# Kernel tuning notes

Measured on AMD Instinct MI355X. Metric: run time of the kernel, lower is better.

## Reference

```python
import jax, jax.numpy as jnp
import numpy as np
import math

DX = DZ = DATTN = DOUT = 1024
LX = LZ = 4096

def setup_inputs() -> dict:
    key = jax.random.key(0)
    ks = jax.random.split(key, 6)
    X = jax.random.normal(ks[0], (DX, LX), dtype=jnp.float32)
    Z = jax.random.normal(ks[1], (DZ, LZ), dtype=jnp.float32)
    mask = jax.random.randint(ks[2], (LZ, LX), 0, 2) > 0  # bool (lz, lx)
    Wq = jax.random.normal(ks[3], (DATTN, DX), dtype=jnp.float32) / math.sqrt(DATTN)
    bq = jnp.zeros((DATTN, 1), dtype=jnp.float32)
    Wk = jax.random.normal(ks[4], (DATTN, DZ), dtype=jnp.float32) / math.sqrt(DATTN)
    bk = jnp.zeros((DATTN, 1), dtype=jnp.float32)
    Wv = jax.random.normal(ks[5], (DOUT, DZ), dtype=jnp.float32) / math.sqrt(DOUT)
    bv = jnp.zeros((DOUT, 1), dtype=jnp.float32)
    return {"X": X, "Z": Z, "mask": mask, "Wq": Wq, "bq": bq,
            "Wk": Wk, "bk": bk, "Wv": Wv, "bv": bv}

def reference(X, Z, mask, Wq, bq, Wk, bk, Wv, bv):
    dattn_sqrt = math.sqrt(Wq.shape[0])
    q = Wq @ X + bq                      # (dattn, lx)
    k = Wk @ Z + bk                      # (dattn, lz)
    v = Wv @ Z + bv                      # (dout, lz)
    score = k.T @ q                      # (lz, lx)
    # masked_fill with -1000 happens BEFORE scaling, matching the original
    score = jnp.where(mask, score, jnp.float32(-1000.0))
    attn = jax.nn.softmax(score / dattn_sqrt, axis=0)  # softmax over lz (dim 0)
    return v @ attn                      # (dout, lx)
```

## Files before the change

### kernel.cpp

```cpp
#include <hip/hip_runtime.h>
#include <hip/hip_bf16.h>
#include <math.h>

constexpr int DXc = 1024;
constexpr int DZc = 1024;
constexpr int LXc = 4096;
constexpr int LZc = 4096;
constexpr int DAc = 1024;
constexpr int DOc = 1024;

typedef __attribute__((ext_vector_type(8))) short bf16x8;
typedef __attribute__((ext_vector_type(4))) float f32x4;

__device__ __forceinline__ ushort f2bf(float f) {
    __hip_bfloat16 h = __float2bfloat16(f);
    return *reinterpret_cast<ushort*>(&h);
}
__device__ __forceinline__ float bflo(unsigned u) {
    return __builtin_bit_cast(float, u << 16);
}
__device__ __forceinline__ float bfhi(unsigned u) {
    return __builtin_bit_cast(float, u & 0xffff0000u);
}

enum BiasMode { BIAS_NONE, BIAS_M, BIAS_N };

template<BiasMode BMODE, bool OUT_BF16, bool SPLIT>
__device__ __forceinline__ void gemm_tile(
    const ushort* __restrict__ A, const ushort* __restrict__ B,
    const float* __restrict__ bias, void* __restrict__ Cv,
    int M, int N, int K, int lda, int ldb, int ldc,
    int m0, int n0, int kbase, int zsplit,
    ushort* As, ushort* Bs)
{
    constexpr int BK = 32;
    const int tid = threadIdx.x;
    const int wv  = tid >> 6;
    const int wm  = (wv >> 1) * 64;
    const int wn  = (wv & 1) * 64;
    const int ln  = tid & 63;
    const int lrow = ln & 15;
    const int quad = ln >> 4;

    const int srow = tid >> 2;
    const int sseg = (tid & 3) * 8;
    const ushort* Ag = A + (size_t)(m0 + srow) * lda + sseg + kbase;
    const ushort* Bg = B + (size_t)(n0 + srow) * ldb + sseg + kbase;
    ushort* AsW = As + wv * 512;
    ushort* BsW = Bs + wv * 512;

    f32x4 acc[4][4] = {};

    for (int k0 = 0; k0 < K; k0 += BK) {
        __syncthreads();
        __builtin_amdgcn_global_load_lds(
            (const __attribute__((address_space(1))) void*)(Ag + k0),
            (__attribute__((address_space(3))) void*)(AsW), 16, 0, 0);
        __builtin_amdgcn_global_load_lds(
            (const __attribute__((address_space(1))) void*)(Ag + (size_t)64 * lda + k0),
            (__attribute__((address_space(3))) void*)(AsW + 2048), 16, 0, 0);
        __builtin_amdgcn_global_load_lds(
            (const __attribute__((address_space(1))) void*)(Bg + k0),
            (__attribute__((address_space(3))) void*)(BsW), 16, 0, 0);
        __builtin_amdgcn_global_load_lds(
            (const __attribute__((address_space(1))) void*)(Bg + (size_t)64 * ldb + k0),
            (__attribute__((address_space(3))) void*)(BsW + 2048), 16, 0, 0);
        __syncthreads();

        bf16x8 af[4], bfr[4];
        #pragma unroll
        for (int t = 0; t < 4; ++t) {
            af[t]  = *reinterpret_cast<const bf16x8*>(&As[(wm + t * 16 + lrow) * BK + quad * 8]);
            bfr[t] = *reinterpret_cast<const bf16x8*>(&Bs[(wn + t * 16 + lrow) * BK + quad * 8]);
        }
        #pragma unroll
        for (int mi = 0; mi < 4; ++mi)
            #pragma unroll
            for (int nj = 0; nj < 4; ++nj)
                acc[mi][nj] = __builtin_amdgcn_mfma_f32_16x16x32_bf16(
                    af[mi], bfr[nj], acc[mi][nj], 0, 0, 0);
    }

    float*  Cf = (float*)Cv + (SPLIT ? (size_t)zsplit * M * ldc : 0);
    ushort* Cb = (ushort*)Cv;
    #pragma unroll
    for (int mi = 0; mi < 4; ++mi) {
        #pragma unroll
        for (int r = 0; r < 4; ++r) {
            const int m = m0 + wm + mi * 16 + quad * 4 + r;
            const float bm = (BMODE == BIAS_M) ? bias[m] : 0.0f;
            #pragma unroll
            for (int nj = 0; nj < 4; ++nj) {
                const int n = n0 + wn + nj * 16 + lrow;
                float v = acc[mi][nj][r] + ((BMODE == BIAS_N) ? bias[n] : bm);
                if (OUT_BF16) Cb[(size_t)m * ldc + n] = f2bf(v);
                else          Cf[(size_t)m * ldc + n] = v;
            }
        }
    }
}

__global__ __launch_bounds__(256)
void proj_kernel(const ushort* __restrict__ XT, const ushort* __restrict__ ZT,
                 const ushort* __restrict__ Wqb, const ushort* __restrict__ Wkb,
                 const ushort* __restrict__ Wvb,
                 const float* __restrict__ bq, const float* __restrict__ bk,
                 const float* __restrict__ bv,
                 ushort* __restrict__ qT, ushort* __restrict__ kT,
                 ushort* __restrict__ vB)
{
    __shared__ __align__(16) ushort As[128 * 32];
    __shared__ __align__(16) ushort Bs[128 * 32];
    int b = blockIdx.x;
    if (b < 256) {
        const int x = b & 7, y = b >> 3;
        gemm_tile<BIAS_N, true, false>(XT, Wqb, bq, qT, LXc, DAc, DXc,
                                       DXc, DXc, DAc, y * 128, x * 128, 0, 0, As, Bs);
    } else if (b < 512) {
        b -= 256;
        const int x = b & 7, y = b >> 3;
        gemm_tile<BIAS_N, true, false>(ZT, Wkb, bk, kT, LZc, DAc, DZc,
                                       DZc, DZc, DAc, y * 128, x * 128, 0, 0, As, Bs);
    } else {
        b -= 512;
        const int x = b & 31, y = b >> 5;
        gemm_tile<BIAS_M, true, false>(Wvb, ZT, bv, vB, DOc, LZc, DZc,
                                       DZc, DZc, LZc, y * 128, x * 128, 0, 0, As, Bs);
    }
}

__global__ __launch_bounds__(256)
void score_kernel(const ushort* __restrict__ qT, const ushort* __restrict__ kT,
                  ushort* __restrict__ sTb)
{
    __shared__ __align__(16) ushort As[128 * 32];
    __shared__ __align__(16) ushort Bs[128 * 32];
    const int b = blockIdx.x;
    const int x = b & 31, y = b >> 5;
    gemm_tile<BIAS_NONE, true, false>(qT, kT, nullptr, sTb, LXc, LZc, DAc,
                                      DAc, DAc, LZc, y * 128, x * 128, 0, 0, As, Bs);
}

__global__ __launch_bounds__(256)
void out_kernel(const ushort* __restrict__ vB, const ushort* __restrict__ sTb,
                float* __restrict__ P)
{
    __shared__ __align__(16) ushort As[128 * 32];
    __shared__ __align__(16) ushort Bs[128 * 32];
    gemm_tile<BIAS_NONE, false, true>(vB, sTb, nullptr, P, DOc, LXc, LZc / 4,
                                      LZc, LZc, LXc,
                                      blockIdx.y * 128, blockIdx.x * 128,
                                      blockIdx.z * (LZc / 4), blockIdx.z, As, Bs);
}

__global__ __launch_bounds__(256)
void prep_kernel(const float* __restrict__ X, const float* __restrict__ Z,
                 const float* __restrict__ Wq, const float* __restrict__ Wk,
                 const float* __restrict__ Wv, const int* __restrict__ mask,
                 ushort* __restrict__ XT, ushort* __restrict__ ZT,
                 ushort* __restrict__ Wqb, ushort* __restrict__ Wkb,
                 ushort* __restrict__ Wvb, unsigned* __restrict__ bits)
{
    __shared__ float tile[32][33];
    const int tid = threadIdx.x;
    int b = blockIdx.x;

    if (b < 8192) {
        const float* in  = (b < 4096) ? X : Z;
        ushort*      out = (b < 4096) ? XT : ZT;
        const int local = b & 4095;
        const int bx = local & 127, by = local >> 7;
        const int c0 = bx * 32, r0 = by * 32;
        const int tx = tid & 31, ty = tid >> 5;
        #pragma unroll
        for (int i = 0; i < 32; i += 8)
            tile[ty + i][tx] = in[(size_t)(r0 + ty + i) * LXc + c0 + tx];
        __syncthreads();
        #pragma unroll
        for (int i = 0; i < 32; i += 8)
            out[(size_t)(c0 + ty + i) * DXc + r0 + tx] = f2bf(tile[tx][ty + i]);
        return;
    }
    if (b < 11264) {
        b -= 8192;
        const float* in  = (b < 1024) ? Wq : (b < 2048) ? Wk : Wv;
        ushort*      out = (b < 1024) ? Wqb : (b < 2048) ? Wkb : Wvb;
        const int local = b & 1023;
        const size_t i = ((size_t)local * 256 + tid) * 4;
        float4 f = *reinterpret_cast<const float4*>(in + i);
        ushort4 u;
        u.x = f2bf(f.x); u.y = f2bf(f.y); u.z = f2bf(f.z); u.w = f2bf(f.w);
        *reinterpret_cast<ushort4*>(out + i) = u;
        return;
    }
    b -= 11264;
    const int xb = b & 15, zb = b >> 4;
    const int x  = xb * 256 + tid;
    const int z0 = zb * 32;
    unsigned w = 0;
    #pragma unroll 8
    for (int i = 0; i < 32; ++i)
        w |= (mask[(size_t)(z0 + i) * LXc + x] != 0 ? 1u : 0u) << i;
    bits[(size_t)x * (LZc / 32) + zb] = w;
}

__global__ __launch_bounds__(256)
void softmax_kernel(ushort* __restrict__ sTb, const unsigned* __restrict__ bits)
{
    const int x   = blockIdx.x;
    const int tid = threadIdx.x;
    ushort* row = sTb + (size_t)x * LZc;
    constexpr float scale = 1.0f / 32.0f;
    constexpr float MASKV = -1000.0f / 32.0f;

    float v[16];
    float mx = -1e30f;
    #pragma unroll
    for (int r = 0; r < 2; ++r) {
        const uint4 pk = *reinterpret_cast<const uint4*>(row + (size_t)(r * 256 + tid) * 8);
        const unsigned* w = reinterpret_cast<const unsigned*>(&pk);
        const unsigned mb = (bits[(size_t)x * 128 + r * 64 + (tid >> 2)] >> ((tid & 3) * 8)) & 0xffu;
        #pragma unroll
        for (int j = 0; j < 4; ++j) {
            const float lo = ((mb >> (2 * j))     & 1u) ? bflo(w[j]) * scale : MASKV;
            const float hi = ((mb >> (2 * j + 1)) & 1u) ? bfhi(w[j]) * scale : MASKV;
            v[r * 8 + 2 * j]     = lo;
            v[r * 8 + 2 * j + 1] = hi;
            mx = fmaxf(mx, fmaxf(lo, hi));
        }
    }
    __shared__ float redmax[4];
    #pragma unroll
    for (int off = 32; off > 0; off >>= 1)
        mx = fmaxf(mx, __shfl_down(mx, off, 64));
    if ((tid & 63) == 0) redmax[tid >> 6] = mx;
    __syncthreads();
    mx = fmaxf(fmaxf(redmax[0], redmax[1]), fmaxf(redmax[2], redmax[3]));

    float sum = 0.0f;
    #pragma unroll
    for (int i = 0; i < 16; ++i) {
        v[i] = __expf(v[i] - mx);
        sum += v[i];
    }
    __shared__ float redsum[4];
    #pragma unroll
    for (int off = 32; off > 0; off >>= 1)
        sum += __shfl_down(sum, off, 64);
    if ((tid & 63) == 0) redsum[tid >> 6] = sum;
    __syncthreads();
    sum = redsum[0] + redsum[1] + redsum[2] + redsum[3];
    const float inv = 1.0f / sum;

    #pragma unroll
    for (int r = 0; r < 2; ++r) {
        uint4 pk;
        unsigned* w = reinterpret_cast<unsigned*>(&pk);
        #pragma unroll
        for (int j = 0; j < 4; ++j) {
            const unsigned lo = f2bf(v[r * 8 + 2 * j] * inv);
            const unsigned hi = f2bf(v[r * 8 + 2 * j + 1] * inv);
            w[j] = lo | (hi << 16);
        }
        *reinterpret_cast<uint4*>(row + (size_t)(r * 256 + tid) * 8) = pk;
    }
}

__global__ __launch_bounds__(256)
void reduce_kernel(const float* __restrict__ P, float* __restrict__ out)
{
    constexpr size_t total = (size_t)DOc * LXc;
    const size_t i = ((size_t)blockIdx.x * 256 + threadIdx.x) * 4;
    float4 s = *reinterpret_cast<const float4*>(P + i);
    #pragma unroll
    for (int p = 1; p < 4; ++p) {
        const float4 t = *reinterpret_cast<const float4*>(P + (size_t)p * total + i);
        s.x += t.x; s.y += t.y; s.z += t.z; s.w += t.w;
    }
    *reinterpret_cast<float4*>(out + i) = s;
}

extern "C" void kernel_launch(void* const* d_in, const int* in_sizes, int n_in,
                              void* d_out, int out_size, void* d_ws, size_t ws_size,
                              hipStream_t stream)
{
    const float* X    = (const float*)d_in[0];
    const float* Z    = (const float*)d_in[1];
    const int*   mask = (const int*)  d_in[2];
    const float* Wq   = (const float*)d_in[3];
    const float* bq   = (const float*)d_in[4];
    const float* Wk   = (const float*)d_in[5];
    const float* bk   = (const float*)d_in[6];
    const float* Wv   = (const float*)d_in[7];
    const float* bv   = (const float*)d_in[8];
    float* out = (float*)d_out;

    char* ws = (char*)d_ws;
    ushort*   XT   = (ushort*)(ws);
    ushort*   ZT   = (ushort*)(ws + ( 8ull << 20));
    ushort*   Wqb  = (ushort*)(ws + (16ull << 20));
    ushort*   Wkb  = (ushort*)(ws + (18ull << 20));
    ushort*   Wvb  = (ushort*)(ws + (20ull << 20));
    ushort*   qT   = (ushort*)(ws + (22ull << 20));
    ushort*   kT   = (ushort*)(ws + (30ull << 20));
    float*    P    = (float*) (ws);
    ushort*   vB   = (ushort*)(ws + (64ull << 20));
    ushort*   sTb  = (ushort*)(ws + (72ull << 20));
    unsigned* bits = (unsigned*)(ws + (104ull << 20));

    prep_kernel<<<dim3(13312), 256, 0, stream>>>(X, Z, Wq, Wk, Wv, mask,
                                                 XT, ZT, Wqb, Wkb, Wvb, bits);
    proj_kernel<<<dim3(768), 256, 0, stream>>>(XT, ZT, Wqb, Wkb, Wvb,
                                               bq, bk, bv, qT, kT, vB);
    score_kernel<<<dim3(1024), 256, 0, stream>>>(qT, kT, sTb);
    softmax_kernel<<<dim3(LXc), 256, 0, stream>>>(sTb, bits);
    out_kernel<<<dim3(32, 8, 4), 256, 0, stream>>>(vB, sTb, P);
    reduce_kernel<<<dim3(DOc * LXc / 1024), 256, 0, stream>>>(P, out);
}
```

Measured before the change: 310.0 us.

## Replace 128x128 GEMM tiles with swizzled 256x256 double-buffered pipelined tiles

Replaces the 128x128, BK=32 GEMM helper with a 256x256, 8-wave kernel. It stages 64-wide K chunks into double-buffered, XOR-swizzled LDS (128 KB dynamic shared memory) and interleaves quarter-tile MFMA batches with async global-to-LDS loads, using explicit waitcnt and barriers plus setprio. The aim is more data reuse per byte loaded, fewer LDS bank conflicts, and global load latency hidden behind MFMA work. In exchange the grids shrink (192/256/256 blocks on a 256-CU part), which risks poor occupancy and wave-quantization, and the hand-written waitcnt schedule is fragile.

```diff
diff --git a/kernel.cpp b/kernel.cpp
--- a/kernel.cpp
+++ b/kernel.cpp
@@ -25,132 +25,217 @@
 
 enum BiasMode { BIAS_NONE, BIAS_M, BIAS_N };
 
+#define SCHED0() __builtin_amdgcn_sched_barrier(0)
+#define BAR2()   do { SCHED0(); __builtin_amdgcn_s_barrier(); SCHED0(); } while (0)
+#define LGKM0()  do { asm volatile("s_waitcnt lgkmcnt(0)" ::: "memory"); SCHED0(); } while (0)
+#define VMCNT(n) do { asm volatile("s_waitcnt vmcnt(" #n ")" ::: "memory"); SCHED0(); } while (0)
+
 template<BiasMode BMODE, bool OUT_BF16, bool SPLIT>
-__device__ __forceinline__ void gemm_tile(
+__device__ __forceinline__ void gemm256(
     const ushort* __restrict__ A, const ushort* __restrict__ B,
     const float* __restrict__ bias, void* __restrict__ Cv,
     int M, int N, int K, int lda, int ldb, int ldc,
-    int m0, int n0, int kbase, int zsplit,
-    ushort* As, ushort* Bs)
-{
-    constexpr int BK = 32;
-    const int tid = threadIdx.x;
-    const int wv  = tid >> 6;
-    const int wm  = (wv >> 1) * 64;
-    const int wn  = (wv & 1) * 64;
-    const int ln  = tid & 63;
-    const int lrow = ln & 15;
-    const int quad = ln >> 4;
-
-    const int srow = tid >> 2;
-    const int sseg = (tid & 3) * 8;
-    const ushort* Ag = A + (size_t)(m0 + srow) * lda + sseg + kbase;
-    const ushort* Bg = B + (size_t)(n0 + srow) * ldb + sseg + kbase;
-    ushort* AsW = As + wv * 512;
-    ushort* BsW = Bs + wv * 512;
-
-    f32x4 acc[4][4] = {};
-
-    for (int k0 = 0; k0 < K; k0 += BK) {
-        __syncthreads();
-        __builtin_amdgcn_global_load_lds(
-            (const __attribute__((address_space(1))) void*)(Ag + k0),
-            (__attribute__((address_space(3))) void*)(AsW), 16, 0, 0);
-        __builtin_amdgcn_global_load_lds(
-            (const __attribute__((address_space(1))) void*)(Ag + (size_t)64 * lda + k0),
-            (__attribute__((address_space(3))) void*)(AsW + 2048), 16, 0, 0);
-        __builtin_amdgcn_global_load_lds(
-            (const __attribute__((address_space(1))) void*)(Bg + k0),
-            (__attribute__((address_space(3))) void*)(BsW), 16, 0, 0);
-        __builtin_amdgcn_global_load_lds(
-            (const __attribute__((address_space(1))) void*)(Bg + (size_t)64 * ldb + k0),
-            (__attribute__((address_space(3))) void*)(BsW + 2048), 16, 0, 0);
-        __syncthreads();
-
-        bf16x8 af[4], bfr[4];
-        #pragma unroll
-        for (int t = 0; t < 4; ++t) {
-            af[t]  = *reinterpret_cast<const bf16x8*>(&As[(wm + t * 16 + lrow) * BK + quad * 8]);
-            bfr[t] = *reinterpret_cast<const bf16x8*>(&Bs[(wn + t * 16 + lrow) * BK + quad * 8]);
-        }
-        #pragma unroll
-        for (int mi = 0; mi < 4; ++mi)
+    int m0, int n0, int kbase, int zsplit, char* smem)
+{
+    const int tid  = threadIdx.x;
+    const int wid  = tid >> 6, lane = tid & 63;
+    const int wr   = wid >> 2, wc = wid & 3;
+    const int lrow = lane & 15, quad = lane >> 4;
+    const int swz  = (lrow & 7) << 4;
+    const int cx0  = (quad * 16) ^ swz;
+    const int cx1  = (64 + quad * 16) ^ swz;
+    const int raB  = (wr * 16 + lrow) * 128;
+    const int rbB  = (wc * 16 + lrow) * 128;
+
+    char* const Ab0 = smem;
+    char* const Ab1 = smem + 32768;
+    char* const Bb0 = smem + 65536;
+    char* const Bb1 = smem + 98304;
+
+    auto stage = [&](const ushort* __restrict__ Mat, int ld, int r0, int kc,
+                     char* dstBuf, int h) {
+        #pragma unroll
+        for (int r = 0; r < 2; ++r) {
+            const int q = h * 16384 + r * 8192 + wid * 1024 + lane * 16;
+            const int p = q ^ (((q >> 7) & 7) << 4);
+            const ushort* g = Mat + (size_t)(r0 + (p >> 7)) * ld + kc + ((p & 127) >> 1);
+            __builtin_amdgcn_global_load_lds(
+                (const __attribute__((address_space(1))) void*)g,
+                (__attribute__((address_space(3))) void*)(dstBuf + h * 16384 + r * 8192 + wid * 1024),
+                16, 0, 0);
+        }
+    };
+
+    f32x4  acc[8][4] = {};
+    bf16x8 alo[4][2], ahi[4][2], blo[2][2], bhi[2][2];
+
+    auto ldLo = [&](char* Abuf, char* Bbuf) {
+        #pragma unroll
+        for (int m = 0; m < 4; ++m) {
+            alo[m][0] = *reinterpret_cast<const bf16x8*>(Abuf + m * 4096 + raB + cx0);
+            alo[m][1] = *reinterpret_cast<const bf16x8*>(Abuf + m * 4096 + raB + cx1);
+        }
+        #pragma unroll
+        for (int n = 0; n < 2; ++n) {
+            blo[n][0] = *reinterpret_cast<const bf16x8*>(Bbuf + n * 8192 + rbB + cx0);
+            blo[n][1] = *reinterpret_cast<const bf16x8*>(Bbuf + n * 8192 + rbB + cx1);
+        }
+    };
+    auto ldAhi = [&](char* Abuf) {
+        #pragma unroll
+        for (int m = 0; m < 4; ++m) {
+            ahi[m][0] = *reinterpret_cast<const bf16x8*>(Abuf + (m + 4) * 4096 + raB + cx0);
+            ahi[m][1] = *reinterpret_cast<const bf16x8*>(Abuf + (m + 4) * 4096 + raB + cx1);
+        }
+    };
+    auto ldBhi = [&](char* Bbuf) {
+        #pragma unroll
+        for (int n = 0; n < 2; ++n) {
+            bhi[n][0] = *reinterpret_cast<const bf16x8*>(Bbuf + (n + 2) * 8192 + rbB + cx0);
+            bhi[n][1] = *reinterpret_cast<const bf16x8*>(Bbuf + (n + 2) * 8192 + rbB + cx1);
+        }
+    };
+    auto mmaQ = [&](bf16x8 (&a)[4][2], bf16x8 (&b)[2][2], int mh, int nh) {
+        __builtin_amdgcn_s_setprio(1);
+        #pragma unroll
+        for (int m = 0; m < 4; ++m)
             #pragma unroll
-            for (int nj = 0; nj < 4; ++nj)
-                acc[mi][nj] = __builtin_amdgcn_mfma_f32_16x16x32_bf16(
-                    af[mi], bfr[nj], acc[mi][nj], 0, 0, 0);
-    }
-
-    float*  Cf = (float*)Cv + (SPLIT ? (size_t)zsplit * M * ldc : 0);
+            for (int n = 0; n < 2; ++n) {
+                f32x4& c = acc[mh * 4 + m][nh * 2 + n];
+                c = __builtin_amdgcn_mfma_f32_16x16x32_bf16(a[m][0], b[n][0], c, 0, 0, 0);
+                c = __builtin_amdgcn_mfma_f32_16x16x32_bf16(a[m][1], b[n][1], c, 0, 0, 0);
+            }
+        __builtin_amdgcn_s_setprio(0);
+    };
+
+    const int NIT = K >> 7;
+
+    stage(A, lda, m0, kbase,      Ab0, 0);
+    stage(B, ldb, n0, kbase,      Bb0, 0);
+    stage(B, ldb, n0, kbase,      Bb0, 1);
+    stage(A, lda, m0, kbase,      Ab0, 1);
+    VMCNT(4);
+    stage(A, lda, m0, kbase + 64, Ab1, 0);
+    stage(B, ldb, n0, kbase + 64, Bb1, 0);
+    stage(B, ldb, n0, kbase + 64, Bb1, 1);
+    VMCNT(6);
+    BAR2();
+
+    #pragma unroll 1
+    for (int it = 0; it < NIT; ++it) {
+        const bool st  = (it < NIT - 1);
+        const int kU   = kbase + (2 * it + 1) * 64;
+        const int kT2  = kbase + (2 * it + 2) * 64;
+        const int kT3  = kbase + (2 * it + 3) * 64;
+
+        ldLo(Ab0, Bb0);
+        stage(A, lda, m0, kU, Ab1, 1);
+        asm volatile("s_waitcnt lgkmcnt(8)" ::: "memory");
+        BAR2(); LGKM0();
+        mmaQ(alo, blo, 0, 0);
+        BAR2();
+        ldBhi(Bb0);
+        if (st) stage(A, lda, m0, kT2, Ab0, 0);
+        BAR2(); LGKM0();
+        mmaQ(alo, bhi, 0, 1);
+        BAR2();
+        ldAhi(Ab0);
+        if (st) stage(B, ldb, n0, kT2, Bb0, 0);
+        BAR2(); LGKM0();
+        mmaQ(ahi, bhi, 1, 1);
+        BAR2();
+        if (st) { stage(B, ldb, n0, kT2, Bb0, 1); VMCNT(6); }
+        else    { VMCNT(0); }
+        BAR2();
+        mmaQ(ahi, blo, 1, 0);
+        BAR2();
+        ldLo(Ab1, Bb1);
+        if (st) stage(A, lda, m0, kT2, Ab0, 1);
+        asm volatile("s_waitcnt lgkmcnt(8)" ::: "memory");
+        BAR2(); LGKM0();
+        mmaQ(alo, blo, 0, 0);
+        BAR2();
+        ldBhi(Bb1);
+        if (st) stage(A, lda, m0, kT3, Ab1, 0);
+        BAR2(); LGKM0();
+        mmaQ(alo, bhi, 0, 1);
+        BAR2();
+        ldAhi(Ab1);
+        if (st) stage(B, ldb, n0, kT3, Bb1, 0);
+        BAR2(); LGKM0();
+        mmaQ(ahi, bhi, 1, 1);
+        BAR2();
+        if (st) { stage(B, ldb, n0, kT3, Bb1, 1); VMCNT(6); }
+        else    { VMCNT(0); }
+        BAR2();
+        mmaQ(ahi, blo, 1, 0);
+        BAR2();
+    }
+
+    float*  Cf = (float*)Cv + (SPLIT ? (size_t)zsplit * (size_t)M * ldc : 0);
     ushort* Cb = (ushort*)Cv;
     #pragma unroll
-    for (int mi = 0; mi < 4; ++mi) {
+    for (int m = 0; m < 8; ++m) {
+        const int rowb = m0 + 32 * m + wr * 16 + quad * 4;
         #pragma unroll
         for (int r = 0; r < 4; ++r) {
-            const int m = m0 + wm + mi * 16 + quad * 4 + r;
-            const float bm = (BMODE == BIAS_M) ? bias[m] : 0.0f;
+            const int row = rowb + r;
+            const float bm = (BMODE == BIAS_M) ? bias[row] : 0.0f;
             #pragma unroll
-            for (int nj = 0; nj < 4; ++nj) {
-                const int n = n0 + wn + nj * 16 + lrow;
-                float v = acc[mi][nj][r] + ((BMODE == BIAS_N) ? bias[n] : bm);
-                if (OUT_BF16) Cb[(size_t)m * ldc + n] = f2bf(v);
-                else          Cf[(size_t)m * ldc + n] = v;
+            for (int n = 0; n < 4; ++n) {
+                const int col = n0 + 64 * n + wc * 16 + lrow;
+                float v = acc[m][n][r] + ((BMODE == BIAS_N) ? bias[col] : bm);
+                if (OUT_BF16) Cb[(size_t)row * ldc + col] = f2bf(v);
+                else          Cf[(size_t)row * ldc + col] = v;
             }
         }
     }
 }
 
-__global__ __launch_bounds__(256)
-void proj_kernel(const ushort* __restrict__ XT, const ushort* __restrict__ ZT,
-                 const ushort* __restrict__ Wqb, const ushort* __restrict__ Wkb,
-                 const ushort* __restrict__ Wvb,
-                 const float* __restrict__ bq, const float* __restrict__ bk,
-                 const float* __restrict__ bv,
-                 ushort* __restrict__ qT, ushort* __restrict__ kT,
-                 ushort* __restrict__ vB)
-{
-    __shared__ __align__(16) ushort As[128 * 32];
-    __shared__ __align__(16) ushort Bs[128 * 32];
+__global__ __launch_bounds__(512, 2)
+void proj256_kernel(const ushort* __restrict__ XT, const ushort* __restrict__ ZT,
+                    const ushort* __restrict__ Wqb, const ushort* __restrict__ Wkb,
+                    const ushort* __restrict__ Wvb,
+                    const float* __restrict__ bq, const float* __restrict__ bk,
+                    const float* __restrict__ bv,
+                    ushort* __restrict__ qT, ushort* __restrict__ kT,
+                    ushort* __restrict__ vB)
+{
+    extern __shared__ char smem[];
     int b = blockIdx.x;
-    if (b < 256) {
-        const int x = b & 7, y = b >> 3;
-        gemm_tile<BIAS_N, true, false>(XT, Wqb, bq, qT, LXc, DAc, DXc,
-                                       DXc, DXc, DAc, y * 128, x * 128, 0, 0, As, Bs);
-    } else if (b < 512) {
-        b -= 256;
-        const int x = b & 7, y = b >> 3;
-        gemm_tile<BIAS_N, true, false>(ZT, Wkb, bk, kT, LZc, DAc, DZc,
-                                       DZc, DZc, DAc, y * 128, x * 128, 0, 0, As, Bs);
+    if (b < 64) {
+        gemm256<BIAS_N, true, false>(XT, Wqb, bq, qT, LXc, DAc, DXc, DXc, DXc, DAc,
+                                     (b >> 2) * 256, (b & 3) * 256, 0, 0, smem);
+    } else if (b < 128) {
+        b -= 64;
+        gemm256<BIAS_N, true, false>(ZT, Wkb, bk, kT, LZc, DAc, DZc, DZc, DZc, DAc,
+                                     (b >> 2) * 256, (b & 3) * 256, 0, 0, smem);
     } else {
-        b -= 512;
-        const int x = b & 31, y = b >> 5;
-        gemm_tile<BIAS_M, true, false>(Wvb, ZT, bv, vB, DOc, LZc, DZc,
-                                       DZc, DZc, LZc, y * 128, x * 128, 0, 0, As, Bs);
-    }
-}
-
-__global__ __launch_bounds__(256)
-void score_kernel(const ushort* __restrict__ qT, const ushort* __restrict__ kT,
-                  ushort* __restrict__ sTb)
-{
-    __shared__ __align__(16) ushort As[128 * 32];
-    __shared__ __align__(16) ushort Bs[128 * 32];
+        b -= 128;
+        gemm256<BIAS_M, true, false>(Wvb, ZT, bv, vB, DOc, LZc, DZc, DZc, DZc, LZc,
+                                     (b >> 4) * 256, (b & 15) * 256, 0, 0, smem);
+    }
+}
+
+__global__ __launch_bounds__(512, 2)
+void score256_kernel(const ushort* __restrict__ qT, const ushort* __restrict__ kT,
+                     ushort* __restrict__ sTb)
+{
+    extern __shared__ char smem[];
     const int b = blockIdx.x;
-    const int x = b & 31, y = b >> 5;
-    gemm_tile<BIAS_NONE, true, false>(qT, kT, nullptr, sTb, LXc, LZc, DAc,
-                                      DAc, DAc, LZc, y * 128, x * 128, 0, 0, As, Bs);
-}
-
-__global__ __launch_bounds__(256)
-void out_kernel(const ushort* __restrict__ vB, const ushort* __restrict__ sTb,
-                float* __restrict__ P)
-{
-    __shared__ __align__(16) ushort As[128 * 32];
-    __shared__ __align__(16) ushort Bs[128 * 32];
-    gemm_tile<BIAS_NONE, false, true>(vB, sTb, nullptr, P, DOc, LXc, LZc / 4,
-                                      LZc, LZc, LXc,
-                                      blockIdx.y * 128, blockIdx.x * 128,
-                                      blockIdx.z * (LZc / 4), blockIdx.z, As, Bs);
+    gemm256<BIAS_NONE, true, false>(qT, kT, nullptr, sTb, LXc, LZc, DAc, DAc, DAc, LZc,
+                                    (b >> 4) * 256, (b & 15) * 256, 0, 0, smem);
+}
+
+__global__ __launch_bounds__(512, 2)
+void out256_kernel(const ushort* __restrict__ vB, const ushort* __restrict__ sTb,
+                   float* __restrict__ P)
+{
+    extern __shared__ char smem[];
+    gemm256<BIAS_NONE, false, true>(vB, sTb, nullptr, P, DOc, LXc, LZc / 4,
+                                    LZc, LZc, LXc,
+                                    blockIdx.y * 256, blockIdx.x * 256,
+                                    blockIdx.z * (LZc / 4), blockIdx.z, smem);
 }
 
 __global__ __launch_bounds__(256)
@@ -294,6 +379,17 @@
     const float* Wv   = (const float*)d_in[7];
     const float* bv   = (const float*)d_in[8];
     float* out = (float*)d_out;
+
+    static bool inited = false;
+    if (!inited) {
+        (void)hipFuncSetAttribute((const void*)proj256_kernel,
+                                  hipFuncAttributeMaxDynamicSharedMemorySize, 131072);
+        (void)hipFuncSetAttribute((const void*)score256_kernel,
+                                  hipFuncAttributeMaxDynamicSharedMemorySize, 131072);
+        (void)hipFuncSetAttribute((const void*)out256_kernel,
+                                  hipFuncAttributeMaxDynamicSharedMemorySize, 131072);
+        inited = true;
+    }
 
     char* ws = (char*)d_ws;
     ushort*   XT   = (ushort*)(ws);
@@ -310,10 +406,10 @@
 
     prep_kernel<<<dim3(13312), 256, 0, stream>>>(X, Z, Wq, Wk, Wv, mask,
                                                  XT, ZT, Wqb, Wkb, Wvb, bits);
-    proj_kernel<<<dim3(768), 256, 0, stream>>>(XT, ZT, Wqb, Wkb, Wvb,
-                                               bq, bk, bv, qT, kT, vB);
-    score_kernel<<<dim3(1024), 256, 0, stream>>>(qT, kT, sTb);
+    proj256_kernel<<<dim3(192), 512, 131072, stream>>>(XT, ZT, Wqb, Wkb, Wvb,
+                                                       bq, bk, bv, qT, kT, vB);
+    score256_kernel<<<dim3(256), 512, 131072, stream>>>(qT, kT, sTb);
     softmax_kernel<<<dim3(LXc), 256, 0, stream>>>(sTb, bits);
-    out_kernel<<<dim3(32, 8, 4), 256, 0, stream>>>(vB, sTb, P);
+    out256_kernel<<<dim3(16, 4, 4), 512, 131072, stream>>>(vB, sTb, P);
     reduce_kernel<<<dim3(DOc * LXc / 1024), 256, 0, stream>>>(P, out);
 }
```

New measurement: 280.5 us. 9.5% less time.
